# Kernel tuning notes

Measured on AMD Instinct MI355X. Metric: run time of the kernel, lower is better.

The kernel has to match this reference:

```python
import jax, jax.numpy as jnp
import numpy as np

B, T, N, E = 4, 8, 512, 8192
CIN, H, HEADS = 64, 128, 4


def setup_inputs() -> dict:
    key = jax.random.key(0)
    ks = jax.random.split(key, 8)
    G = B * T
    s = 0.05
    return {
        "x": jax.random.normal(ks[0], (G, N, CIN), jnp.float32),
        "edge_index": jax.random.randint(ks[1], (G, 2, E), 0, N, dtype=jnp.int64),
        "W1": jax.random.normal(ks[2], (CIN, H), jnp.float32) * s,
        "b1": jnp.zeros((H,), jnp.float32),
        "W2": jax.random.normal(ks[3], (H, H), jnp.float32) * s,
        "b2": jnp.zeros((H,), jnp.float32),
        "in_proj_w": jax.random.normal(ks[4], (3 * H, H), jnp.float32) * s,
        "in_proj_b": jnp.zeros((3 * H,), jnp.float32),
        "out_proj_w": jax.random.normal(ks[5], (H, H), jnp.float32) * s,
        "out_proj_b": jnp.zeros((H,), jnp.float32),
    }


def gcn_layer(x, src, dst, W, b, num_nodes):
    # PyG GCNConv: add self-loops, sym-normalize deg^-1/2[src]*deg^-1/2[dst]
    xl = x @ W                                            # [GN, H]
    deg = jax.ops.segment_sum(jnp.ones_like(dst, dtype=xl.dtype), dst,
                              num_segments=num_nodes) + 1.0  # +1 self-loop
    dinv = jax.lax.rsqrt(deg)
    norm = dinv[src] * dinv[dst]                          # [Etot]
    agg = jax.ops.segment_sum(xl[src] * norm[:, None], dst, num_segments=num_nodes)
    agg = agg + xl * (dinv * dinv)[:, None]               # self-loop term
    return agg + b


def reference(x, edge_index, W1, b1, W2, b2, in_proj_w, in_proj_b, out_proj_w, out_proj_b):
    G, n, cin = x.shape
    GN = G * n
    offs = (jnp.arange(G, dtype=edge_index.dtype) * n)[:, None]  # disjoint union
    src = (edge_index[:, 0, :] + offs).reshape(-1)
    dst = (edge_index[:, 1, :] + offs).reshape(-1)
    xf = x.reshape(GN, cin)
    h = gcn_layer(xf, src, dst, W1, b1, GN)
    h = gcn_layer(h, src, dst, W2, b2, GN)
    hc = h.shape[-1]
    h = h.reshape(B, T * n, hc)                           # [B, S, H]
    # torch.nn.MultiheadAttention with packed qkv in_proj
    qkv = h @ in_proj_w.T + in_proj_b
    q, k, v = jnp.split(qkv, 3, axis=-1)
    hd = hc // HEADS
    def sh(t):
        return t.reshape(B, -1, HEADS, hd).transpose(0, 2, 1, 3)  # [B,h,S,d]
    q, k, v = sh(q), sh(k), sh(v)
    att = jax.nn.softmax(jnp.einsum('bhqd,bhkd->bhqk', q, k) / jnp.sqrt(jnp.float32(hd)), axis=-1)
    o = jnp.einsum('bhqk,bhkd->bhqd', att, v).transpose(0, 2, 1, 3).reshape(B, -1, hc)
    return o @ out_proj_w.T + out_proj_b
```

## Files before the change

### kernel.cpp

```cpp
#include <hip/hip_runtime.h>
#include <hip/hip_bf16.h>

#define G     32
#define NPG   512
#define EPG   8192
#define GN    16384
#define ETOT  (G*EPG)
#define CIN   64
#define H     128
#define NB    4
#define S     4096
#define HEADS 4
#define HD    32
#define QKV   384

typedef __attribute__((ext_vector_type(8))) short short8;
typedef __attribute__((ext_vector_type(4))) float floatx4;

__device__ __forceinline__ float bf16_to_f32(unsigned short u) {
    unsigned int x = ((unsigned int)u) << 16;
    return __uint_as_float(x);
}
__device__ __forceinline__ unsigned short f32_to_bf16(float f) {
    __hip_bfloat16 h = (__hip_bfloat16)f;
    return *(unsigned short*)&h;
}
__device__ __forceinline__ float ldf(const void* p, long i, int f32) {
    return f32 ? ((const float*)p)[i] : bf16_to_f32(((const unsigned short*)p)[i]);
}

__global__ void detect_kernel(const unsigned short* __restrict__ xraw,
                              const int* __restrict__ eiraw, int* __restrict__ flags) {
    __shared__ float smax[256];
    __shared__ int   sor[256];
    int t = threadIdx.x;
    float m = 0.f;
    for (int i = t; i < 4096; i += 256)
        m = fmaxf(m, fabsf(bf16_to_f32(xraw[i])));
    int orv = 0;
    for (int i = t; i < 2048; i += 256)
        orv |= eiraw[2 * i + 1];
    smax[t] = m; sor[t] = orv;
    __syncthreads();
    for (int off = 128; off > 0; off >>= 1) {
        if (t < off) {
            smax[t] = fmaxf(smax[t], smax[t + off]);
            sor[t] |= sor[t + off];
        }
        __syncthreads();
    }
    if (t == 0) {
        flags[0] = (smax[0] > 1000.f) ? 1 : 0;
        flags[1] = (sor[0] == 0) ? 1 : 0;
    }
}

#define XN   (GN*CIN)
#define E1   (XN + H*CIN)
#define E2   (E1 + H*H)
#define E3   (E2 + QKV*H)
#define E4   (E3 + H*H)
#define E5   (E4 + H)
#define E6   (E5 + H)
#define E7   (E6 + QKV)
#define CTOT (E7 + H)
__global__ void conv_all_kernel(const void* x_raw, const void* W1_raw, const void* b1_raw,
                                const void* W2_raw, const void* b2_raw, const void* Wq_raw,
                                const void* bq_raw, const void* Wo_raw, const void* bo_raw,
                                unsigned short* __restrict__ xb,
                                unsigned short* __restrict__ W1T,
                                unsigned short* __restrict__ W2T,
                                unsigned short* __restrict__ Wqb,
                                unsigned short* __restrict__ Wob,
                                float* __restrict__ b1f, float* __restrict__ b2f,
                                float* __restrict__ bqf, float* __restrict__ bof,
                                const int* __restrict__ flags) {
    int i = blockIdx.x * blockDim.x + threadIdx.x;
    if (i >= CTOT) return;
    int f32 = flags[0];
    if (i < XN) {
        xb[i] = f32_to_bf16(ldf(x_raw, i, f32));
    } else if (i < E1) {
        int j = i - XN, c = j / CIN, r = j - c * CIN;
        W1T[j] = f32_to_bf16(ldf(W1_raw, (long)r * H + c, f32));
    } else if (i < E2) {
        int j = i - E1, c = j >> 7, r = j & 127;
        W2T[j] = f32_to_bf16(ldf(W2_raw, (long)r * H + c, f32));
    } else if (i < E3) {
        int j = i - E2;
        Wqb[j] = f32_to_bf16(ldf(Wq_raw, j, f32));
    } else if (i < E4) {
        int j = i - E3;
        Wob[j] = f32_to_bf16(ldf(Wo_raw, j, f32));
    } else if (i < E5) { b1f[i - E4] = ldf(b1_raw, i - E4, f32); }
    else if (i < E6) { b2f[i - E5] = ldf(b2_raw, i - E5, f32); }
    else if (i < E7) { bqf[i - E6] = ldf(bq_raw, i - E6, f32); }
    else             { bof[i - E7] = ldf(bo_raw, i - E7, f32); }
}

__global__ void edges_kernel(const int* __restrict__ ei, int* __restrict__ srcA,
                             int* __restrict__ dstA, const int* __restrict__ flags) {
    int t = blockIdx.x * blockDim.x + threadIdx.x;
    if (t >= ETOT) return;
    int g = t >> 13, e = t & (EPG - 1);
    int sh = flags[1];
    long long si = ((long long)(g * 2 + 0) * EPG + e) << sh;
    long long di = ((long long)(g * 2 + 1) * EPG + e) << sh;
    srcA[t] = g * NPG + ei[si];
    dstA[t] = g * NPG + ei[di];
}

__global__ void count_kernel(const int* __restrict__ dstA, int* __restrict__ cnt) {
    int t = blockIdx.x * blockDim.x + threadIdx.x;
    if (t >= ETOT) return;
    atomicAdd(&cnt[dstA[t]], 1);
}

__global__ void scan_kernel(const int* __restrict__ cnt, int* __restrict__ row_start,
                            int* __restrict__ fill_pos, float* __restrict__ dinv) {
    __shared__ int tmp[NPG];
    int g = blockIdx.x, t = threadIdx.x;
    int c = cnt[g * NPG + t];
    tmp[t] = c;
    __syncthreads();
    for (int off = 1; off < NPG; off <<= 1) {
        int v = (t >= off) ? tmp[t - off] : 0;
        __syncthreads();
        tmp[t] += v;
        __syncthreads();
    }
    int excl = tmp[t] - c;
    int rs = g * EPG + excl;
    row_start[g * NPG + t] = rs;
    fill_pos[g * NPG + t]  = rs;
    dinv[g * NPG + t] = 1.0f / sqrtf((float)c + 1.0f);
}

__global__ void fill_kernel(const int* __restrict__ srcA, const int* __restrict__ dstA,
                            int* __restrict__ fill_pos, int* __restrict__ csr_src) {
    int t = blockIdx.x * blockDim.x + threadIdx.x;
    if (t >= ETOT) return;
    int pos = atomicAdd(&fill_pos[dstA[t]], 1);
    csr_src[pos] = srcA[t];
}

template<int KD>
__global__ __launch_bounds__(256) void mm_gcn_kernel(const unsigned short* __restrict__ A,
        const unsigned short* __restrict__ B, const float* __restrict__ dinv,
        unsigned short* __restrict__ Y) {
    int tid = threadIdx.x, wave = tid >> 6, lane = tid & 63, m = lane & 15, quad = lane >> 4;
    int row0 = blockIdx.x * 64 + wave * 16;
    floatx4 acc[8] = {};
    for (int kc = 0; kc < KD; kc += 32) {
        short8 af = *(const short8*)&A[(size_t)(row0 + m) * KD + kc + quad * 8];
#pragma unroll
        for (int t = 0; t < 8; t++) {
            short8 bf = *(const short8*)&B[(size_t)(t * 16 + m) * KD + kc + quad * 8];
            acc[t] = __builtin_amdgcn_mfma_f32_16x16x32_bf16(af, bf, acc[t], 0, 0, 0);
        }
    }
    int rbase = row0 + quad * 4;
    float4 dv4 = *(const float4*)&dinv[rbase];
    float dv[4] = {dv4.x, dv4.y, dv4.z, dv4.w};
#pragma unroll
    for (int t = 0; t < 8; t++) {
        int col = t * 16 + m;
#pragma unroll
        for (int r = 0; r < 4; r++)
            Y[(size_t)(rbase + r) * H + col] = f32_to_bf16(acc[t][r] * dv[r]);
    }
}

__global__ void agg_kernel(const unsigned short* __restrict__ y,
                           const int* __restrict__ row_start, const int* __restrict__ cnt,
                           const int* __restrict__ csr_src, const float* __restrict__ dinv,
                           const float* __restrict__ bias, unsigned short* __restrict__ hout) {
    int i = blockIdx.x;
    int c = threadIdx.x;
    float acc = bf16_to_f32(y[(size_t)i * H + c]);
    int rs = row_start[i], n = cnt[i];
    int p = 0;
    for (; p + 4 <= n; p += 4) {
        int s0 = csr_src[rs + p + 0];
        int s1 = csr_src[rs + p + 1];
        int s2 = csr_src[rs + p + 2];
        int s3 = csr_src[rs + p + 3];
        float a0 = bf16_to_f32(y[(size_t)s0 * H + c]);
        float a1 = bf16_to_f32(y[(size_t)s1 * H + c]);
        float a2 = bf16_to_f32(y[(size_t)s2 * H + c]);
        float a3 = bf16_to_f32(y[(size_t)s3 * H + c]);
        acc += (a0 + a1) + (a2 + a3);
    }
    for (; p < n; p++)
        acc += bf16_to_f32(y[(size_t)csr_src[rs + p] * H + c]);
    hout[(size_t)i * H + c] = f32_to_bf16(acc * dinv[i] + bias[c]);
}

__global__ __launch_bounds__(256) void mmqkv_kernel(const unsigned short* __restrict__ A,
        const unsigned short* __restrict__ B, const float* __restrict__ bias,
        unsigned short* __restrict__ Qx, unsigned short* __restrict__ Kx,
        unsigned short* __restrict__ Vtx) {
    int tid = threadIdx.x, wave = tid >> 6, lane = tid & 63, m = lane & 15, quad = lane >> 4;
    int row0 = blockIdx.x * 64 + wave * 16;
    floatx4 acc[24] = {};
    for (int kc = 0; kc < H; kc += 32) {
        short8 af = *(const short8*)&A[(size_t)(row0 + m) * H + kc + quad * 8];
#pragma unroll
        for (int t = 0; t < 24; t++) {
            short8 bf = *(const short8*)&B[(size_t)(t * 16 + m) * H + kc + quad * 8];
            acc[t] = __builtin_amdgcn_mfma_f32_16x16x32_bf16(af, bf, acc[t], 0, 0, 0);
        }
    }
    int rbase = row0 + quad * 4;
    int b = rbase >> 12, s0 = rbase & (S - 1);
#pragma unroll
    for (int t = 0; t < 24; t++) {
        int j = t * 16 + m;
        float bj = bias[j];
        int jj = j & 127, head = jj >> 5, hd = jj & 31;
        int bh = b * HEADS + head;
        if (t < 8) {
#pragma unroll
            for (int r = 0; r < 4; r++)
                Qx[((size_t)bh * S + s0 + r) * HD + hd] =
                    f32_to_bf16((acc[t][r] + bj) * 0.17677669529663687f);
        } else if (t < 16) {
#pragma unroll
            for (int r = 0; r < 4; r++)
                Kx[((size_t)bh * S + s0 + r) * HD + hd] = f32_to_bf16(acc[t][r] + bj);
        } else {
#pragma unroll
            for (int r = 0; r < 4; r++)
                Vtx[((size_t)bh * HD + hd) * S + s0 + r] = f32_to_bf16(acc[t][r] + bj);
        }
    }
}

__global__ __launch_bounds__(256) void attn3_kernel(
        const unsigned short* __restrict__ Qx, const unsigned short* __restrict__ Kx,
        const unsigned short* __restrict__ Vtx, unsigned short* __restrict__ Ob) {
    __shared__ unsigned short Psh[2][4][2][2][16][24];

    int tid = threadIdx.x, wave = tid >> 6, lane = tid & 63;
    int m = lane & 15, quad = lane >> 4;
    int bh = blockIdx.z * HEADS + blockIdx.y;
    const unsigned short* Qb  = Qx  + (size_t)bh * S * HD;
    const unsigned short* Kb  = Kx  + (size_t)bh * S * HD;
    const unsigned short* Vtb = Vtx + (size_t)bh * HD * S;

    int q0 = blockIdx.x * 128 + wave * 32;
    short8 qa = *(const short8*)&Qb[(size_t)(q0 + m) * HD + quad * 8];
    short8 qb = *(const short8*)&Qb[(size_t)(q0 + 16 + m) * HD + quad * 8];

    floatx4 oa0 = {}, oa1 = {}, ob0 = {}, ob1 = {};
    float la0 = 0.f, la1 = 0.f, la2 = 0.f, la3 = 0.f;
    float lb0 = 0.f, lb1 = 0.f, lb2 = 0.f, lb3 = 0.f;
    short8 pfa = {}, pfb = {};
    short8 vp0 = {}, vp1 = {};

    short8 kf0 = *(const short8*)&Kb[(size_t)m * HD + quad * 8];
    short8 kf1 = *(const short8*)&Kb[(size_t)(m + 16) * HD + quad * 8];
    short8 vc0 = *(const short8*)&Vtb[(size_t)m * S + quad * 8];
    short8 vc1 = *(const short8*)&Vtb[(size_t)(m + 16) * S + quad * 8];

    int rdoff = (quad >> 1) * 384 + m * 24 + (quad & 1) * 8;
    int qr = quad * 4;

    for (int i = 0; i < S / 32; i++) {
        floatx4 z = {};
        floatx4 sa0 = __builtin_amdgcn_mfma_f32_16x16x32_bf16(qa, kf0, z, 0, 0, 0);
        floatx4 sa1 = __builtin_amdgcn_mfma_f32_16x16x32_bf16(qa, kf1, z, 0, 0, 0);
        floatx4 sb0 = __builtin_amdgcn_mfma_f32_16x16x32_bf16(qb, kf0, z, 0, 0, 0);
        floatx4 sb1 = __builtin_amdgcn_mfma_f32_16x16x32_bf16(qb, kf1, z, 0, 0, 0);

        if (i > 0) {
            asm volatile("s_waitcnt lgkmcnt(0)" ::: "memory");
            const unsigned short* Pr = &Psh[(i - 1) & 1][wave][0][0][0][0];
            pfa = *(const short8*)&Pr[rdoff];
            pfb = *(const short8*)&Pr[768 + rdoff];
        }

        float pa00 = __expf(sa0[0]), pa01 = __expf(sa0[1]),
              pa02 = __expf(sa0[2]), pa03 = __expf(sa0[3]);
        float pa10 = __expf(sa1[0]), pa11 = __expf(sa1[1]),
              pa12 = __expf(sa1[2]), pa13 = __expf(sa1[3]);
        float pb00 = __expf(sb0[0]), pb01 = __expf(sb0[1]),
              pb02 = __expf(sb0[2]), pb03 = __expf(sb0[3]);
        float pb10 = __expf(sb1[0]), pb11 = __expf(sb1[1]),
              pb12 = __expf(sb1[2]), pb13 = __expf(sb1[3]);
        la0 += pa00 + pa10; la1 += pa01 + pa11;
        la2 += pa02 + pa12; la3 += pa03 + pa13;
        lb0 += pb00 + pb10; lb1 += pb01 + pb11;
        lb2 += pb02 + pb12; lb3 += pb03 + pb13;

        unsigned short* Pw = &Psh[i & 1][wave][0][0][0][0];
        Pw[(qr + 0) * 24 + m]       = f32_to_bf16(pa00);
        Pw[(qr + 1) * 24 + m]       = f32_to_bf16(pa01);
        Pw[(qr + 2) * 24 + m]       = f32_to_bf16(pa02);
        Pw[(qr + 3) * 24 + m]       = f32_to_bf16(pa03);
        Pw[384 + (qr + 0) * 24 + m] = f32_to_bf16(pa10);
        Pw[384 + (qr + 1) * 24 + m] = f32_to_bf16(pa11);
        Pw[384 + (qr + 2) * 24 + m] = f32_to_bf16(pa12);
        Pw[384 + (qr + 3) * 24 + m] = f32_to_bf16(pa13);
        Pw[768 + (qr + 0) * 24 + m]       = f32_to_bf16(pb00);
        Pw[768 + (qr + 1) * 24 + m]       = f32_to_bf16(pb01);
        Pw[768 + (qr + 2) * 24 + m]       = f32_to_bf16(pb02);
        Pw[768 + (qr + 3) * 24 + m]       = f32_to_bf16(pb03);
        Pw[768 + 384 + (qr + 0) * 24 + m] = f32_to_bf16(pb10);
        Pw[768 + 384 + (qr + 1) * 24 + m] = f32_to_bf16(pb11);
        Pw[768 + 384 + (qr + 2) * 24 + m] = f32_to_bf16(pb12);
        Pw[768 + 384 + (qr + 3) * 24 + m] = f32_to_bf16(pb13);

        if (i > 0) {
            oa0 = __builtin_amdgcn_mfma_f32_16x16x32_bf16(pfa, vp0, oa0, 0, 0, 0);
            oa1 = __builtin_amdgcn_mfma_f32_16x16x32_bf16(pfa, vp1, oa1, 0, 0, 0);
            ob0 = __builtin_amdgcn_mfma_f32_16x16x32_bf16(pfb, vp0, ob0, 0, 0, 0);
            ob1 = __builtin_amdgcn_mfma_f32_16x16x32_bf16(pfb, vp1, ob1, 0, 0, 0);
        }

        vp0 = vc0; vp1 = vc1;
        int ktn = ((i + 1) * 32) & (S - 1);
        kf0 = *(const short8*)&Kb[(size_t)(ktn + m) * HD + quad * 8];
        kf1 = *(const short8*)&Kb[(size_t)(ktn + m + 16) * HD + quad * 8];
        vc0 = *(const short8*)&Vtb[(size_t)m * S + ktn + quad * 8];
        vc1 = *(const short8*)&Vtb[(size_t)(m + 16) * S + ktn + quad * 8];
    }

    asm volatile("s_waitcnt lgkmcnt(0)" ::: "memory");
    const unsigned short* Pr = &Psh[(S / 32 - 1) & 1][wave][0][0][0][0];
    pfa = *(const short8*)&Pr[rdoff];
    pfb = *(const short8*)&Pr[768 + rdoff];
    oa0 = __builtin_amdgcn_mfma_f32_16x16x32_bf16(pfa, vp0, oa0, 0, 0, 0);
    oa1 = __builtin_amdgcn_mfma_f32_16x16x32_bf16(pfa, vp1, oa1, 0, 0, 0);
    ob0 = __builtin_amdgcn_mfma_f32_16x16x32_bf16(pfb, vp0, ob0, 0, 0, 0);
    ob1 = __builtin_amdgcn_mfma_f32_16x16x32_bf16(pfb, vp1, ob1, 0, 0, 0);

#pragma unroll
    for (int off = 1; off < 16; off <<= 1) {
        la0 += __shfl_xor(la0, off); la1 += __shfl_xor(la1, off);
        la2 += __shfl_xor(la2, off); la3 += __shfl_xor(la3, off);
        lb0 += __shfl_xor(lb0, off); lb1 += __shfl_xor(lb1, off);
        lb2 += __shfl_xor(lb2, off); lb3 += __shfl_xor(lb3, off);
    }
    float ia[4] = {1.f / la0, 1.f / la1, 1.f / la2, 1.f / la3};
    float ib[4] = {1.f / lb0, 1.f / lb1, 1.f / lb2, 1.f / lb3};
    float A0[4] = {oa0[0], oa0[1], oa0[2], oa0[3]};
    float A1[4] = {oa1[0], oa1[1], oa1[2], oa1[3]};
    float B0[4] = {ob0[0], ob0[1], ob0[2], ob0[3]};
    float B1[4] = {ob1[0], ob1[1], ob1[2], ob1[3]};

    int growa = blockIdx.z * S + q0 + quad * 4;
    int col = blockIdx.y * HD + m;
#pragma unroll
    for (int r = 0; r < 4; r++) {
        Ob[(size_t)(growa + r) * H + col]           = f32_to_bf16(A0[r] * ia[r]);
        Ob[(size_t)(growa + r) * H + col + 16]      = f32_to_bf16(A1[r] * ia[r]);
        Ob[(size_t)(growa + 16 + r) * H + col]      = f32_to_bf16(B0[r] * ib[r]);
        Ob[(size_t)(growa + 16 + r) * H + col + 16] = f32_to_bf16(B1[r] * ib[r]);
    }
}

__global__ __launch_bounds__(256) void mmout_kernel(const unsigned short* __restrict__ A,
        const unsigned short* __restrict__ B, const float* __restrict__ bias,
        void* __restrict__ out, const int* __restrict__ flags) {
    int tid = threadIdx.x, wave = tid >> 6, lane = tid & 63, m = lane & 15, quad = lane >> 4;
    int row0 = blockIdx.x * 64 + wave * 16;
    floatx4 acc[8] = {};
    for (int kc = 0; kc < H; kc += 32) {
        short8 af = *(const short8*)&A[(size_t)(row0 + m) * H + kc + quad * 8];
#pragma unroll
        for (int t = 0; t < 8; t++) {
            short8 bf = *(const short8*)&B[(size_t)(t * 16 + m) * H + kc + quad * 8];
            acc[t] = __builtin_amdgcn_mfma_f32_16x16x32_bf16(af, bf, acc[t], 0, 0, 0);
        }
    }
    int rbase = row0 + quad * 4;
    int f32o = flags[0];
#pragma unroll
    for (int t = 0; t < 8; t++) {
        int col = t * 16 + m;
        float bj = bias[col];
#pragma unroll
        for (int r = 0; r < 4; r++) {
            float v = acc[t][r] + bj;
            if (f32o) ((float*)out)[(size_t)(rbase + r) * H + col] = v;
            else ((unsigned short*)out)[(size_t)(rbase + r) * H + col] = f32_to_bf16(v);
        }
    }
}

extern "C" void kernel_launch(void* const* d_in, const int* in_sizes, int n_in,
                              void* d_out, int out_size, void* d_ws, size_t ws_size,
                              hipStream_t stream) {
    const void* x_raw    = d_in[0];
    const int*  ei_raw   = (const int*)d_in[1];
    const void* W1_raw   = d_in[2];
    const void* b1_raw   = d_in[3];
    const void* W2_raw   = d_in[4];
    const void* b2_raw   = d_in[5];
    const void* Wq_raw   = d_in[6];
    const void* bq_raw   = d_in[7];
    const void* Wo_raw   = d_in[8];
    const void* bo_raw   = d_in[9];

    char* ws = (char*)d_ws;
    size_t o = 0;
    auto alloc = [&](size_t bytes) { void* p = ws + o; o += (bytes + 1023) & ~1023ull; return p; };

    int*   flags     = (int*)  alloc(1024);
    int*   cnt       = (int*)  alloc((size_t)GN * 4);
    int*   row_start = (int*)  alloc((size_t)GN * 4);
    int*   fill_pos  = (int*)  alloc((size_t)GN * 4);
    float* dinv      = (float*)alloc((size_t)GN * 4);
    int*   srcA      = (int*)  alloc((size_t)ETOT * 4);
    int*   dstA      = (int*)  alloc((size_t)ETOT * 4);
    int*   csr_src   = (int*)  alloc((size_t)ETOT * 4);
    unsigned short* xb   = (unsigned short*)alloc((size_t)GN * CIN * 2);
    unsigned short* W1T  = (unsigned short*)alloc((size_t)H * CIN * 2);
    unsigned short* W2T  = (unsigned short*)alloc((size_t)H * H * 2);
    unsigned short* Wqb  = (unsigned short*)alloc((size_t)QKV * H * 2);
    unsigned short* Wob  = (unsigned short*)alloc((size_t)H * H * 2);
    float* b1f = (float*)alloc(H * 4);
    float* b2f = (float*)alloc(H * 4);
    float* bqf = (float*)alloc(QKV * 4);
    float* bof = (float*)alloc(H * 4);
    unsigned short* y_bf = (unsigned short*)alloc((size_t)GN * H * 2);
    unsigned short* h_bf = (unsigned short*)alloc((size_t)GN * H * 2);
    unsigned short* Qx   = (unsigned short*)alloc((size_t)16 * S * HD * 2);
    unsigned short* Kx   = (unsigned short*)alloc((size_t)16 * S * HD * 2);
    unsigned short* Vtx  = (unsigned short*)alloc((size_t)16 * S * HD * 2);
    unsigned short* Obf  = y_bf;

    detect_kernel<<<1, 256, 0, stream>>>((const unsigned short*)x_raw, ei_raw, flags);

    conv_all_kernel<<<(CTOT + 255) / 256, 256, 0, stream>>>(
        x_raw, W1_raw, b1_raw, W2_raw, b2_raw, Wq_raw, bq_raw, Wo_raw, bo_raw,
        xb, W1T, W2T, Wqb, Wob, b1f, b2f, bqf, bof, flags);

    edges_kernel<<<ETOT / 256, 256, 0, stream>>>(ei_raw, srcA, dstA, flags);
    hipMemsetAsync(cnt, 0, (size_t)GN * 4, stream);
    count_kernel<<<ETOT / 256, 256, 0, stream>>>(dstA, cnt);
    scan_kernel<<<G, NPG, 0, stream>>>(cnt, row_start, fill_pos, dinv);
    fill_kernel<<<ETOT / 256, 256, 0, stream>>>(srcA, dstA, fill_pos, csr_src);

    mm_gcn_kernel<CIN><<<GN / 64, 256, 0, stream>>>(xb, W1T, dinv, y_bf);
    agg_kernel<<<GN, H, 0, stream>>>(y_bf, row_start, cnt, csr_src, dinv, b1f, h_bf);
    mm_gcn_kernel<H><<<GN / 64, 256, 0, stream>>>(h_bf, W2T, dinv, y_bf);
    agg_kernel<<<GN, H, 0, stream>>>(y_bf, row_start, cnt, csr_src, dinv, b2f, h_bf);

    mmqkv_kernel<<<GN / 64, 256, 0, stream>>>(h_bf, Wqb, bqf, Qx, Kx, Vtx);
    attn3_kernel<<<dim3(S / 128, HEADS, NB), 256, 0, stream>>>(Qx, Kx, Vtx, Obf);
    mmout_kernel<<<GN / 64, 256, 0, stream>>>(Obf, Wob, bof, d_out, flags);
}
```

Before: 269.7 us.

## Keep attention probabilities in registers via transposed QK and lane permutes

```diff
diff --git a/kernel.cpp b/kernel.cpp
--- a/kernel.cpp
+++ b/kernel.cpp
@@ -223,7 +223,8 @@
 #pragma unroll
             for (int r = 0; r < 4; r++)
                 Qx[((size_t)bh * S + s0 + r) * HD + hd] =
-                    f32_to_bf16((acc[t][r] + bj) * 0.17677669529663687f);
+                    f32_to_bf16((acc[t][r] + bj) *
+                                (0.17677669529663687f * 1.4426950408889634f));
         } else if (t < 16) {
 #pragma unroll
             for (int r = 0; r < 4; r++)
@@ -236,11 +237,9 @@
     }
 }
 
-__global__ __launch_bounds__(256) void attn3_kernel(
+__global__ __launch_bounds__(256) void attn4_kernel(
         const unsigned short* __restrict__ Qx, const unsigned short* __restrict__ Kx,
         const unsigned short* __restrict__ Vtx, unsigned short* __restrict__ Ob) {
-    __shared__ unsigned short Psh[2][4][2][2][16][24];
-
     int tid = threadIdx.x, wave = tid >> 6, lane = tid & 63;
     int m = lane & 15, quad = lane >> 4;
     int bh = blockIdx.z * HEADS + blockIdx.y;
@@ -253,110 +252,87 @@
     short8 qb = *(const short8*)&Qb[(size_t)(q0 + 16 + m) * HD + quad * 8];
 
     floatx4 oa0 = {}, oa1 = {}, ob0 = {}, ob1 = {};
-    float la0 = 0.f, la1 = 0.f, la2 = 0.f, la3 = 0.f;
-    float lb0 = 0.f, lb1 = 0.f, lb2 = 0.f, lb3 = 0.f;
-    short8 pfa = {}, pfb = {};
-    short8 vp0 = {}, vp1 = {};
+    floatx4 la = {}, lb = {};
+
+    short8 ones = {16256, 16256, 16256, 16256, 16256, 16256, 16256, 16256};
 
     short8 kf0 = *(const short8*)&Kb[(size_t)m * HD + quad * 8];
     short8 kf1 = *(const short8*)&Kb[(size_t)(m + 16) * HD + quad * 8];
     short8 vc0 = *(const short8*)&Vtb[(size_t)m * S + quad * 8];
     short8 vc1 = *(const short8*)&Vtb[(size_t)(m + 16) * S + quad * 8];
 
-    int rdoff = (quad >> 1) * 384 + m * 24 + (quad & 1) * 8;
-    int qr = quad * 4;
-
     for (int i = 0; i < S / 32; i++) {
         floatx4 z = {};
-        floatx4 sa0 = __builtin_amdgcn_mfma_f32_16x16x32_bf16(qa, kf0, z, 0, 0, 0);
-        floatx4 sa1 = __builtin_amdgcn_mfma_f32_16x16x32_bf16(qa, kf1, z, 0, 0, 0);
-        floatx4 sb0 = __builtin_amdgcn_mfma_f32_16x16x32_bf16(qb, kf0, z, 0, 0, 0);
-        floatx4 sb1 = __builtin_amdgcn_mfma_f32_16x16x32_bf16(qb, kf1, z, 0, 0, 0);
-
-        if (i > 0) {
-            asm volatile("s_waitcnt lgkmcnt(0)" ::: "memory");
-            const unsigned short* Pr = &Psh[(i - 1) & 1][wave][0][0][0][0];
-            pfa = *(const short8*)&Pr[rdoff];
-            pfb = *(const short8*)&Pr[768 + rdoff];
-        }
-
-        float pa00 = __expf(sa0[0]), pa01 = __expf(sa0[1]),
-              pa02 = __expf(sa0[2]), pa03 = __expf(sa0[3]);
-        float pa10 = __expf(sa1[0]), pa11 = __expf(sa1[1]),
-              pa12 = __expf(sa1[2]), pa13 = __expf(sa1[3]);
-        float pb00 = __expf(sb0[0]), pb01 = __expf(sb0[1]),
-              pb02 = __expf(sb0[2]), pb03 = __expf(sb0[3]);
-        float pb10 = __expf(sb1[0]), pb11 = __expf(sb1[1]),
-              pb12 = __expf(sb1[2]), pb13 = __expf(sb1[3]);
-        la0 += pa00 + pa10; la1 += pa01 + pa11;
-        la2 += pa02 + pa12; la3 += pa03 + pa13;
-        lb0 += pb00 + pb10; lb1 += pb01 + pb11;
-        lb2 += pb02 + pb12; lb3 += pb03 + pb13;
-
-        unsigned short* Pw = &Psh[i & 1][wave][0][0][0][0];
-        Pw[(qr + 0) * 24 + m]       = f32_to_bf16(pa00);
-        Pw[(qr + 1) * 24 + m]       = f32_to_bf16(pa01);
-        Pw[(qr + 2) * 24 + m]       = f32_to_bf16(pa02);
-        Pw[(qr + 3) * 24 + m]       = f32_to_bf16(pa03);
-        Pw[384 + (qr + 0) * 24 + m] = f32_to_bf16(pa10);
-        Pw[384 + (qr + 1) * 24 + m] = f32_to_bf16(pa11);
-        Pw[384 + (qr + 2) * 24 + m] = f32_to_bf16(pa12);
-        Pw[384 + (qr + 3) * 24 + m] = f32_to_bf16(pa13);
-        Pw[768 + (qr + 0) * 24 + m]       = f32_to_bf16(pb00);
-        Pw[768 + (qr + 1) * 24 + m]       = f32_to_bf16(pb01);
-        Pw[768 + (qr + 2) * 24 + m]       = f32_to_bf16(pb02);
-        Pw[768 + (qr + 3) * 24 + m]       = f32_to_bf16(pb03);
-        Pw[768 + 384 + (qr + 0) * 24 + m] = f32_to_bf16(pb10);
-        Pw[768 + 384 + (qr + 1) * 24 + m] = f32_to_bf16(pb11);
-        Pw[768 + 384 + (qr + 2) * 24 + m] = f32_to_bf16(pb12);
-        Pw[768 + 384 + (qr + 3) * 24 + m] = f32_to_bf16(pb13);
-
-        if (i > 0) {
-            oa0 = __builtin_amdgcn_mfma_f32_16x16x32_bf16(pfa, vp0, oa0, 0, 0, 0);
-            oa1 = __builtin_amdgcn_mfma_f32_16x16x32_bf16(pfa, vp1, oa1, 0, 0, 0);
-            ob0 = __builtin_amdgcn_mfma_f32_16x16x32_bf16(pfb, vp0, ob0, 0, 0, 0);
-            ob1 = __builtin_amdgcn_mfma_f32_16x16x32_bf16(pfb, vp1, ob1, 0, 0, 0);
-        }
-
-        vp0 = vc0; vp1 = vc1;
+        floatx4 ta0 = __builtin_amdgcn_mfma_f32_16x16x32_bf16(kf0, qa, z, 0, 0, 0);
+        floatx4 ta1 = __builtin_amdgcn_mfma_f32_16x16x32_bf16(kf1, qa, z, 0, 0, 0);
+        floatx4 tb0 = __builtin_amdgcn_mfma_f32_16x16x32_bf16(kf0, qb, z, 0, 0, 0);
+        floatx4 tb1 = __builtin_amdgcn_mfma_f32_16x16x32_bf16(kf1, qb, z, 0, 0, 0);
+
+        short8 vp0 = vc0, vp1 = vc1;
         int ktn = ((i + 1) * 32) & (S - 1);
         kf0 = *(const short8*)&Kb[(size_t)(ktn + m) * HD + quad * 8];
         kf1 = *(const short8*)&Kb[(size_t)(ktn + m + 16) * HD + quad * 8];
         vc0 = *(const short8*)&Vtb[(size_t)m * S + ktn + quad * 8];
         vc1 = *(const short8*)&Vtb[(size_t)(m + 16) * S + ktn + quad * 8];
-    }
-
-    asm volatile("s_waitcnt lgkmcnt(0)" ::: "memory");
-    const unsigned short* Pr = &Psh[(S / 32 - 1) & 1][wave][0][0][0][0];
-    pfa = *(const short8*)&Pr[rdoff];
-    pfb = *(const short8*)&Pr[768 + rdoff];
-    oa0 = __builtin_amdgcn_mfma_f32_16x16x32_bf16(pfa, vp0, oa0, 0, 0, 0);
-    oa1 = __builtin_amdgcn_mfma_f32_16x16x32_bf16(pfa, vp1, oa1, 0, 0, 0);
-    ob0 = __builtin_amdgcn_mfma_f32_16x16x32_bf16(pfb, vp0, ob0, 0, 0, 0);
-    ob1 = __builtin_amdgcn_mfma_f32_16x16x32_bf16(pfb, vp1, ob1, 0, 0, 0);
-
-#pragma unroll
-    for (int off = 1; off < 16; off <<= 1) {
-        la0 += __shfl_xor(la0, off); la1 += __shfl_xor(la1, off);
-        la2 += __shfl_xor(la2, off); la3 += __shfl_xor(la3, off);
-        lb0 += __shfl_xor(lb0, off); lb1 += __shfl_xor(lb1, off);
-        lb2 += __shfl_xor(lb2, off); lb3 += __shfl_xor(lb3, off);
-    }
-    float ia[4] = {1.f / la0, 1.f / la1, 1.f / la2, 1.f / la3};
-    float ib[4] = {1.f / lb0, 1.f / lb1, 1.f / lb2, 1.f / lb3};
-    float A0[4] = {oa0[0], oa0[1], oa0[2], oa0[3]};
-    float A1[4] = {oa1[0], oa1[1], oa1[2], oa1[3]};
-    float B0[4] = {ob0[0], ob0[1], ob0[2], ob0[3]};
-    float B1[4] = {ob1[0], ob1[1], ob1[2], ob1[3]};
-
-    int growa = blockIdx.z * S + q0 + quad * 4;
+
+        float pa0 = __builtin_amdgcn_exp2f(ta0[0]);
+        float pa1 = __builtin_amdgcn_exp2f(ta0[1]);
+        float pa2 = __builtin_amdgcn_exp2f(ta0[2]);
+        float pa3 = __builtin_amdgcn_exp2f(ta0[3]);
+        float pa4 = __builtin_amdgcn_exp2f(ta1[0]);
+        float pa5 = __builtin_amdgcn_exp2f(ta1[1]);
+        float pa6 = __builtin_amdgcn_exp2f(ta1[2]);
+        float pa7 = __builtin_amdgcn_exp2f(ta1[3]);
+        float pb0 = __builtin_amdgcn_exp2f(tb0[0]);
+        float pb1 = __builtin_amdgcn_exp2f(tb0[1]);
+        float pb2 = __builtin_amdgcn_exp2f(tb0[2]);
+        float pb3 = __builtin_amdgcn_exp2f(tb0[3]);
+        float pb4 = __builtin_amdgcn_exp2f(tb1[0]);
+        float pb5 = __builtin_amdgcn_exp2f(tb1[1]);
+        float pb6 = __builtin_amdgcn_exp2f(tb1[2]);
+        float pb7 = __builtin_amdgcn_exp2f(tb1[3]);
+
+        unsigned int wa0, wa1, wa2, wa3, wb0, wb1, wb2, wb3;
+        asm("v_cvt_pk_bf16_f32 %0, %1, %2" : "=v"(wa0) : "v"(pa0), "v"(pa1));
+        asm("v_cvt_pk_bf16_f32 %0, %1, %2" : "=v"(wa1) : "v"(pa2), "v"(pa3));
+        asm("v_cvt_pk_bf16_f32 %0, %1, %2" : "=v"(wa2) : "v"(pa4), "v"(pa5));
+        asm("v_cvt_pk_bf16_f32 %0, %1, %2" : "=v"(wa3) : "v"(pa6), "v"(pa7));
+        asm("v_cvt_pk_bf16_f32 %0, %1, %2" : "=v"(wb0) : "v"(pb0), "v"(pb1));
+        asm("v_cvt_pk_bf16_f32 %0, %1, %2" : "=v"(wb1) : "v"(pb2), "v"(pb3));
+        asm("v_cvt_pk_bf16_f32 %0, %1, %2" : "=v"(wb2) : "v"(pb4), "v"(pb5));
+        asm("v_cvt_pk_bf16_f32 %0, %1, %2" : "=v"(wb3) : "v"(pb6), "v"(pb7));
+
+        asm("v_permlane32_swap_b32 %0, %1" : "+v"(wa0), "+v"(wa2));
+        asm("v_permlane32_swap_b32 %0, %1" : "+v"(wa1), "+v"(wa3));
+        asm("v_permlane16_swap_b32 %0, %1" : "+v"(wa0), "+v"(wa2));
+        asm("v_permlane16_swap_b32 %0, %1" : "+v"(wa1), "+v"(wa3));
+        asm("v_permlane32_swap_b32 %0, %1" : "+v"(wb0), "+v"(wb2));
+        asm("v_permlane32_swap_b32 %0, %1" : "+v"(wb1), "+v"(wb3));
+        asm("v_permlane16_swap_b32 %0, %1" : "+v"(wb0), "+v"(wb2));
+        asm("v_permlane16_swap_b32 %0, %1" : "+v"(wb1), "+v"(wb3));
+
+        union PW { unsigned int u[4]; short8 s8; };
+        PW pwa, pwb;
+        pwa.u[0] = wa0; pwa.u[1] = wa1; pwa.u[2] = wa2; pwa.u[3] = wa3;
+        pwb.u[0] = wb0; pwb.u[1] = wb1; pwb.u[2] = wb2; pwb.u[3] = wb3;
+
+        oa0 = __builtin_amdgcn_mfma_f32_16x16x32_bf16(pwa.s8, vp0, oa0, 0, 0, 0);
+        oa1 = __builtin_amdgcn_mfma_f32_16x16x32_bf16(pwa.s8, vp1, oa1, 0, 0, 0);
+        la  = __builtin_amdgcn_mfma_f32_16x16x32_bf16(pwa.s8, ones, la, 0, 0, 0);
+        ob0 = __builtin_amdgcn_mfma_f32_16x16x32_bf16(pwb.s8, vp0, ob0, 0, 0, 0);
+        ob1 = __builtin_amdgcn_mfma_f32_16x16x32_bf16(pwb.s8, vp1, ob1, 0, 0, 0);
+        lb  = __builtin_amdgcn_mfma_f32_16x16x32_bf16(pwb.s8, ones, lb, 0, 0, 0);
+    }
+
+    int grow = blockIdx.z * S + q0 + quad * 4;
     int col = blockIdx.y * HD + m;
 #pragma unroll
     for (int r = 0; r < 4; r++) {
-        Ob[(size_t)(growa + r) * H + col]           = f32_to_bf16(A0[r] * ia[r]);
-        Ob[(size_t)(growa + r) * H + col + 16]      = f32_to_bf16(A1[r] * ia[r]);
-        Ob[(size_t)(growa + 16 + r) * H + col]      = f32_to_bf16(B0[r] * ib[r]);
-        Ob[(size_t)(growa + 16 + r) * H + col + 16] = f32_to_bf16(B1[r] * ib[r]);
+        float iar = 1.f / la[r], ibr = 1.f / lb[r];
+        Ob[(size_t)(grow + r) * H + col]           = f32_to_bf16(oa0[r] * iar);
+        Ob[(size_t)(grow + r) * H + col + 16]      = f32_to_bf16(oa1[r] * iar);
+        Ob[(size_t)(grow + 16 + r) * H + col]      = f32_to_bf16(ob0[r] * ibr);
+        Ob[(size_t)(grow + 16 + r) * H + col + 16] = f32_to_bf16(ob1[r] * ibr);
     }
 }
 
@@ -449,6 +425,6 @@
     agg_kernel<<<GN, H, 0, stream>>>(y_bf, row_start, cnt, csr_src, dinv, b2f, h_bf);
 
     mmqkv_kernel<<<GN / 64, 256, 0, stream>>>(h_bf, Wqb, bqf, Qx, Kx, Vtx);
-    attn3_kernel<<<dim3(S / 128, HEADS, NB), 256, 0, stream>>>(Qx, Kx, Vtx, Obf);
+    attn4_kernel<<<dim3(S / 128, HEADS, NB), 256, 0, stream>>>(Qx, Kx, Vtx, Obf);
     mmout_kernel<<<GN / 64, 256, 0, stream>>>(Obf, Wob, bof, d_out, flags);
 }
```

New measurement: 269.5 us. Within noise of the previous version (-0.1%).
